# Kernel tuning notes

Measured on AMD Instinct MI355X. Metric: run time of the kernel, lower is better.

## Reference

```python
import jax, jax.numpy as jnp
import numpy as np

HEADS = 4
LOCAL_CTX = 8  # local_attn_ctx (stride)


def _strided_transpose(x, n_ctx, local_ctx):
    # [B, n_ctx, E] -> reshape [B, n_ctx//local, local, E] -> swap -> [B, n_ctx, E]
    B, _, E = x.shape
    bT = n_ctx // local_ctx
    return x.reshape(B, bT, local_ctx, E).transpose(0, 2, 1, 3).reshape(B, n_ctx, E)


def _strided_untranspose(a, n_ctx, local_ctx):
    B, _, E = a.shape
    bT = n_ctx // local_ctx
    return a.reshape(B, local_ctx, bT, E).transpose(0, 2, 1, 3).reshape(B, n_ctx, E)


def setup_inputs() -> dict:
    key = jax.random.key(0)
    ks = jax.random.split(key, 6)
    B, T, E = 2048, 64, 256
    value = jax.random.normal(ks[0], (B, T, E), dtype=jnp.float32)
    k_in = jax.random.normal(ks[1], (B, T, E), dtype=jnp.float32)
    query = jax.random.normal(ks[2], (B, T, E), dtype=jnp.float32)
    mask = jnp.ones((B, T), dtype=jnp.int32)  # unused by the block
    W_ff = jax.random.normal(ks[3], (256, T * E), dtype=jnp.float32) * (1.0 / np.sqrt(T * E))
    b_ff = jax.random.normal(ks[4], (256,), dtype=jnp.float32) * 0.01
    return {"value": value, "key": k_in, "query": query, "mask": mask, "W_ff": W_ff, "b_ff": b_ff}


def reference(value, key, query, mask, W_ff, b_ff):
    B, n_ctx, E = query.shape
    # strided transpose of q, k, v
    q = _strided_transpose(query, n_ctx, LOCAL_CTX)
    k = _strided_transpose(key, n_ctx, LOCAL_CTX)
    v = _strided_transpose(value, n_ctx, LOCAL_CTX)
    scale = 1.0 / np.sqrt(E // HEADS)  # n_state = embd // heads
    w = jax.nn.softmax(jnp.einsum('bqe,bke->bqk', q, k) * scale, axis=-1)
    a = jnp.einsum('bqk,bke->bqe', w, v)
    attention = _strided_untranspose(a, n_ctx, LOCAL_CTX)
    # residual + dropout (eval-mode identity)
    x = attention + query
    # flatten-linear + ReLU
    out = jax.nn.relu(x.reshape(B, n_ctx * E) @ W_ff.T + b_ff)
    return (out, attention)
```

## Files before the change

### kernel.cpp

```cpp
#include <hip/hip_runtime.h>
#include <stdint.h>

typedef __attribute__((ext_vector_type(8))) short s16x8;
typedef __attribute__((ext_vector_type(4))) float f32x4;

__device__ __forceinline__ unsigned short f2bf(float f) {
  unsigned int u = __float_as_uint(f);
  u += 0x7fffu + ((u >> 16) & 1u);
  return (unsigned short)(u >> 16);
}
__device__ __forceinline__ float bf2f(unsigned short h) {
  return __uint_as_float(((unsigned int)h) << 16);
}
__device__ __forceinline__ unsigned short hi_trunc(float f) {
  return (unsigned short)(__float_as_uint(f) >> 16);
}
__device__ __forceinline__ f32x4 mfma16(s16x8 a, s16x8 b, f32x4 c) {
  return __builtin_amdgcn_mfma_f32_16x16x32_bf16(a, b, c, 0, 0, 0);
}

__global__ __launch_bounds__(256, 4) void attn_kernel(
    const float* __restrict__ Vg, const float* __restrict__ Kg,
    const float* __restrict__ Qg, float* __restrict__ attn_out,
    unsigned short* __restrict__ xb ) {
  __shared__ __align__(16) char smem[40960];
  char* PLB = smem + 32768;

  const int b = blockIdx.x;
  const int tid = threadIdx.x;
  const int lane = tid & 63;
  const int w = tid >> 6;
  const int n = lane & 15;
  const int q = lane >> 4;

  const float* Qb = Qg + (size_t)b * 64 * 256;
  const float* Kb = Kg + (size_t)b * 64 * 256;
  const float* Vb = Vg + (size_t)b * 64 * 256;

  const int ve = tid & 127;
  const int vt0 = tid >> 7;

  f32x4 accS[4];
#pragma unroll
  for (int c = 0; c < 4; ++c) accS[c] = f32x4{0.f, 0.f, 0.f, 0.f};

  for (int ph = 0; ph < 2; ++ph) {
    const int e0 = ph * 128;
    float vr[4][8];
#pragma unroll
    for (int i = 0; i < 4; ++i) {
      int tg = i * 2 + vt0;
#pragma unroll
      for (int j = 0; j < 8; ++j) vr[i][j] = Vb[(tg * 8 + j) * 256 + e0 + ve];
    }
#pragma unroll
    for (int kk = 0; kk < 4; ++kk) {
      const int cb = kk * 32 + q * 8;
      const float* qsrc = Qb + (16 * w + n) * 256 + e0 + cb;
      float4 q0 = *(const float4*)qsrc;
      float4 q1 = *(const float4*)(qsrc + 4);
      float4 k0[4], k1[4];
#pragma unroll
      for (int c = 0; c < 4; ++c) {
        const float* ksrc = Kb + (16 * c + n) * 256 + e0 + cb;
        k0[c] = *(const float4*)ksrc;
        k1[c] = *(const float4*)(ksrc + 4);
      }
      float qa[8] = {q0.x, q0.y, q0.z, q0.w, q1.x, q1.y, q1.z, q1.w};
      s16x8 qh, ql;
#pragma unroll
      for (int j = 0; j < 8; ++j) {
        unsigned short h = hi_trunc(qa[j]);
        qh[j] = (short)h;
        ql[j] = (short)f2bf(qa[j] - bf2f(h));
      }
#pragma unroll
      for (int c = 0; c < 4; ++c) {
        float ka[8] = {k0[c].x, k0[c].y, k0[c].z, k0[c].w,
                       k1[c].x, k1[c].y, k1[c].z, k1[c].w};
        s16x8 kh, kl;
#pragma unroll
        for (int j = 0; j < 8; ++j) {
          unsigned short h = hi_trunc(ka[j]);
          kh[j] = (short)h;
          kl[j] = (short)f2bf(ka[j] - bf2f(h));
        }
        accS[c] = mfma16(qh, kh, accS[c]);
        accS[c] = mfma16(qh, kl, accS[c]);
        accS[c] = mfma16(ql, kh, accS[c]);
      }
    }
#pragma unroll
    for (int i = 0; i < 4; ++i) {
      int tg = i * 2 + vt0;
      int e = e0 + ve;
      s16x8 pk;
#pragma unroll
      for (int j = 0; j < 8; ++j) pk[j] = (short)f2bf(vr[i][j]);
      *(s16x8*)(smem + e * 128 + ((tg * 16) ^ ((e & 7) << 4))) = pk;
    }
  }

  const float scale = 0.125f;
  float p[4][4];
#pragma unroll
  for (int r = 0; r < 4; ++r) {
    float m = -1e30f;
#pragma unroll
    for (int c = 0; c < 4; ++c) m = fmaxf(m, accS[c][r]);
#pragma unroll
    for (int mk = 1; mk < 16; mk <<= 1) m = fmaxf(m, __shfl_xor(m, mk, 64));
    float s = 0.f;
#pragma unroll
    for (int c = 0; c < 4; ++c) {
      float e = __expf((accS[c][r] - m) * scale);
      p[c][r] = e;
      s += e;
    }
#pragma unroll
    for (int mk = 1; mk < 16; mk <<= 1) s += __shfl_xor(s, mk, 64);
    float inv = 1.0f / s;
#pragma unroll
    for (int c = 0; c < 4; ++c) p[c][r] *= inv;
  }

#pragma unroll
  for (int r = 0; r < 4; ++r) {
    int row = 16 * w + 4 * q + r;
    int sw = (row & 7) << 4;
#pragma unroll
    for (int c = 0; c < 4; ++c)
      *(unsigned short*)(PLB + row * 128 + ((2 * (16 * c + n)) ^ sw)) =
          f2bf(p[c][r]);
  }
  __syncthreads();

  f32x4 accA[16];
#pragma unroll
  for (int c = 0; c < 16; ++c) accA[c] = f32x4{0.f, 0.f, 0.f, 0.f};
  __builtin_amdgcn_s_setprio(1);
#pragma unroll
  for (int ks = 0; ks < 2; ++ks) {
    const int cb = (ks * 32 + q * 8) * 2;
    const int sw = (n & 7) << 4;
    s16x8 af = *(const s16x8*)(PLB + (16 * w + n) * 128 + (cb ^ sw));
#pragma unroll
    for (int c = 0; c < 16; ++c) {
      int row = 16 * c + n;
      s16x8 bf = *(const s16x8*)(smem + row * 128 + (cb ^ sw));
      accA[c] = mfma16(af, bf, accA[c]);
    }
  }
  __builtin_amdgcn_s_setprio(0);

  if (xb) {
#pragma unroll
    for (int h = 0; h < 2; ++h) {
      __syncthreads();
#pragma unroll
      for (int r = 0; r < 4; ++r) {
        int t = 16 * w + 4 * q + r;
        int sw = (t & 7) << 4;
#pragma unroll
        for (int c8 = 0; c8 < 8; ++c8) {
          int el = 16 * c8 + n;
          *(float*)(smem + t * 512 + ((el * 4) ^ sw)) = accA[h * 8 + c8][r];
        }
      }
      __syncthreads();
#pragma unroll
      for (int i = 0; i < 8; ++i) {
        int f4 = i * 256 + tid;
        int row = f4 >> 5;
        int col4 = f4 & 31;
        int e = h * 128 + col4 * 4;
        float4 av = *(const float4*)(smem + row * 512 + ((col4 * 16) ^ ((row & 7) << 4)));
        float4 qv = *(const float4*)(Qb + row * 256 + e);
        size_t base = ((size_t)b * 64 + row) * 256 + e;
        *(float4*)(attn_out + base) = av;
        ushort4 o;
        o.x = f2bf(av.x + qv.x);
        o.y = f2bf(av.y + qv.y);
        o.z = f2bf(av.z + qv.z);
        o.w = f2bf(av.w + qv.w);
        *(ushort4*)(xb + base) = o;
      }
    }
  } else {
#pragma unroll
    for (int r = 0; r < 4; ++r) {
      int t = 16 * w + 4 * q + r;
      size_t base = ((size_t)b * 64 + t) * 256;
#pragma unroll
      for (int c = 0; c < 16; ++c) attn_out[base + 16 * c + n] = accA[c][r];
    }
  }
}

__global__ __launch_bounds__(256) void w2b_kernel(const float* __restrict__ W,
                                                  unsigned short* __restrict__ Wb) {
  int i = blockIdx.x * 256 + threadIdx.x;
  float4 v = ((const float4*)W)[i];
  ushort4 o;
  o.x = f2bf(v.x); o.y = f2bf(v.y); o.z = f2bf(v.z); o.w = f2bf(v.w);
  ((ushort4*)Wb)[i] = o;
}

template <bool USE_XB>
__global__ __launch_bounds__(256) void ff_kernel(
    const unsigned short* __restrict__ xb, const float* __restrict__ attn,
    const float* __restrict__ query, const unsigned short* __restrict__ Wb,
    float* __restrict__ part, int kchunk) {
  __shared__ __align__(16) unsigned short As[64 * 72];
  __shared__ __align__(16) unsigned short Bs[64 * 72];
  const int tid = threadIdx.x;
  const int lane = tid & 63, w = tid >> 6, n = lane & 15, q = lane >> 4;
  const int m0 = blockIdx.x * 64;
  const int n0 = blockIdx.y * 64;
  const int k0 = blockIdx.z * kchunk;

  f32x4 acc[4];
#pragma unroll
  for (int c = 0; c < 4; ++c) acc[c] = f32x4{0.f, 0.f, 0.f, 0.f};

  const int srow = tid >> 3;
  const int scol = (tid & 7) * 8;

  for (int kk = 0; kk < kchunk; kk += 64) {
#pragma unroll
    for (int rr = 0; rr < 2; ++rr) {
      int row = rr * 32 + srow;
      size_t ga = (size_t)(m0 + row) * 16384 + k0 + kk + scol;
      if (USE_XB) {
        *(uint4*)(As + row * 72 + scol) = *(const uint4*)(xb + ga);
      } else {
        float4 a0 = *(const float4*)(attn + ga);
        float4 a1 = *(const float4*)(attn + ga + 4);
        float4 q0 = *(const float4*)(query + ga);
        float4 q1 = *(const float4*)(query + ga + 4);
        ushort4 h0, h1;
        h0.x = f2bf(a0.x + q0.x); h0.y = f2bf(a0.y + q0.y);
        h0.z = f2bf(a0.z + q0.z); h0.w = f2bf(a0.w + q0.w);
        h1.x = f2bf(a1.x + q1.x); h1.y = f2bf(a1.y + q1.y);
        h1.z = f2bf(a1.z + q1.z); h1.w = f2bf(a1.w + q1.w);
        *(ushort4*)(As + row * 72 + scol) = h0;
        *(ushort4*)(As + row * 72 + scol + 4) = h1;
      }
      size_t gw = (size_t)(n0 + row) * 16384 + k0 + kk + scol;
      *(uint4*)(Bs + row * 72 + scol) = *(const uint4*)(Wb + gw);
    }
    __syncthreads();
#pragma unroll
    for (int ks = 0; ks < 2; ++ks) {
      const int colb = ks * 32 + q * 8;
      s16x8 af = *(const s16x8*)(As + (16 * w + n) * 72 + colb);
#pragma unroll
      for (int c = 0; c < 4; ++c) {
        s16x8 bf = *(const s16x8*)(Bs + (16 * c + n) * 72 + colb);
        acc[c] = mfma16(af, bf, acc[c]);
      }
    }
    __syncthreads();
  }
#pragma unroll
  for (int r = 0; r < 4; ++r) {
    int m = m0 + 16 * w + 4 * q + r;
#pragma unroll
    for (int c = 0; c < 4; ++c) {
      int nn = n0 + 16 * c + n;
      part[((size_t)blockIdx.z * 2048 + m) * 256 + nn] = acc[c][r];
    }
  }
}

__global__ __launch_bounds__(256) void relu_kernel(const float* __restrict__ part,
                                                   const float* __restrict__ bias,
                                                   float* __restrict__ out, int KS) {
  int idx = blockIdx.x * 256 + threadIdx.x;
  float s = bias[idx & 255];
  for (int ks = 0; ks < KS; ++ks) s += part[(size_t)ks * 2048 * 256 + idx];
  out[idx] = fmaxf(s, 0.f);
}

extern "C" void kernel_launch(void* const* d_in, const int* in_sizes, int n_in,
                              void* d_out, int out_size, void* d_ws, size_t ws_size,
                              hipStream_t stream) {
  const float* value = (const float*)d_in[0];
  const float* key   = (const float*)d_in[1];
  const float* query = (const float*)d_in[2];
  const float* W_ff  = (const float*)d_in[4];
  const float* b_ff  = (const float*)d_in[5];

  float* out  = (float*)d_out;
  float* attn = out + (size_t)2048 * 256;

  const int KS = 4;
  const size_t wb_bytes   = (size_t)256 * 16384 * 2;
  const size_t part_bytes = (size_t)KS * 2048 * 256 * 4;
  const size_t xb_bytes   = (size_t)2048 * 64 * 256 * 2;
  unsigned short* Wb = (unsigned short*)d_ws;
  float* part = (float*)((char*)d_ws + wb_bytes);
  bool use_xb = ws_size >= wb_bytes + part_bytes + xb_bytes;
  unsigned short* xb =
      use_xb ? (unsigned short*)((char*)d_ws + wb_bytes + part_bytes) : nullptr;

  w2b_kernel<<<4096, 256, 0, stream>>>(W_ff, Wb);
  attn_kernel<<<2048, 256, 0, stream>>>(value, key, query, attn, xb);
  dim3 gb(32, 4, KS);
  if (use_xb)
    ff_kernel<true><<<gb, 256, 0, stream>>>(xb, nullptr, nullptr, Wb, part, 16384 / KS);
  else
    ff_kernel<false><<<gb, 256, 0, stream>>>(nullptr, attn, query, Wb, part, 16384 / KS);
  relu_kernel<<<2048, 256, 0, stream>>>(part, b_ff, out, KS);
}
```

Before: 317.3 us.

## Stream V through smaller LDS in quarter chunks and write outputs directly

The attention kernel no longer stages all of V (bf16) in a 32KB LDS buffer. It loads V in four 64-column quarters into an 8KB buffer, prefetching the next quarters into registers while the PV MFMAs for the current quarter run. The epilogue drops the LDS transpose and writes attn_out and the bf16 residual directly with per-element stores. LDS use falls from 40KB to 16KB and the min-blocks launch bound is removed, which should raise occupancy. The cost is extra barriers per quarter and narrower, less coalesced global stores.

```diff
diff --git a/kernel.cpp b/kernel.cpp
--- a/kernel.cpp
+++ b/kernel.cpp
@@ -19,12 +19,24 @@
   return __builtin_amdgcn_mfma_f32_16x16x32_bf16(a, b, c, 0, 0, 0);
 }
 
-__global__ __launch_bounds__(256, 4) void attn_kernel(
+__device__ __forceinline__ void write_vq(char* VqB, int ep2, int tg, const float2* g) {
+  s16x8 lo, hi;
+#pragma unroll
+  for (int j = 0; j < 8; ++j) {
+    lo[j] = (short)f2bf(g[j].x);
+    hi[j] = (short)f2bf(g[j].y);
+  }
+  *(s16x8*)(VqB + ep2 * 128 + ((16 * tg) ^ (((ep2 >> 1) & 7) << 4))) = lo;
+  *(s16x8*)(VqB + (ep2 + 1) * 128 + ((16 * tg) ^ (((ep2 >> 1) & 7) << 4))) = hi;
+}
+
+__global__ __launch_bounds__(256) void attn_kernel(
     const float* __restrict__ Vg, const float* __restrict__ Kg,
     const float* __restrict__ Qg, float* __restrict__ attn_out,
     unsigned short* __restrict__ xb ) {
-  __shared__ __align__(16) char smem[40960];
-  char* PLB = smem + 32768;
+  __shared__ __align__(16) char smem[16384];
+  char* VqB = smem;
+  char* PLB = smem + 8192;
 
   const int b = blockIdx.x;
   const int tid = threadIdx.x;
@@ -37,22 +49,16 @@
   const float* Kb = Kg + (size_t)b * 64 * 256;
   const float* Vb = Vg + (size_t)b * 64 * 256;
 
-  const int ve = tid & 127;
-  const int vt0 = tid >> 7;
+  const int ep2 = (tid & 31) * 2;
+  const int tg = tid >> 5;
 
   f32x4 accS[4];
 #pragma unroll
   for (int c = 0; c < 4; ++c) accS[c] = f32x4{0.f, 0.f, 0.f, 0.f};
 
+#pragma unroll
   for (int ph = 0; ph < 2; ++ph) {
     const int e0 = ph * 128;
-    float vr[4][8];
-#pragma unroll
-    for (int i = 0; i < 4; ++i) {
-      int tg = i * 2 + vt0;
-#pragma unroll
-      for (int j = 0; j < 8; ++j) vr[i][j] = Vb[(tg * 8 + j) * 256 + e0 + ve];
-    }
 #pragma unroll
     for (int kk = 0; kk < 4; ++kk) {
       const int cb = kk * 32 + q * 8;
@@ -90,16 +96,15 @@
         accS[c] = mfma16(ql, kh, accS[c]);
       }
     }
-#pragma unroll
-    for (int i = 0; i < 4; ++i) {
-      int tg = i * 2 + vt0;
-      int e = e0 + ve;
-      s16x8 pk;
-#pragma unroll
-      for (int j = 0; j < 8; ++j) pk[j] = (short)f2bf(vr[i][j]);
-      *(s16x8*)(smem + e * 128 + ((tg * 16) ^ ((e & 7) << 4))) = pk;
-    }
-  }
+    if (ph == 0) {
+    }
+  }
+
+  float2 g0[8], g1[8];
+#pragma unroll
+  for (int j = 0; j < 8; ++j) g0[j] = *(const float2*)(Vb + (tg * 8 + j) * 256 + 0 + ep2);
+#pragma unroll
+  for (int j = 0; j < 8; ++j) g1[j] = *(const float2*)(Vb + (tg * 8 + j) * 256 + 64 + ep2);
 
   const float scale = 0.125f;
   float p[4][4];
@@ -133,66 +138,61 @@
       *(unsigned short*)(PLB + row * 128 + ((2 * (16 * c + n)) ^ sw)) =
           f2bf(p[c][r]);
   }
+
+  write_vq(VqB, ep2, tg, g0);
   __syncthreads();
 
-  f32x4 accA[16];
-#pragma unroll
-  for (int c = 0; c < 16; ++c) accA[c] = f32x4{0.f, 0.f, 0.f, 0.f};
-  __builtin_amdgcn_s_setprio(1);
-#pragma unroll
-  for (int ks = 0; ks < 2; ++ks) {
-    const int cb = (ks * 32 + q * 8) * 2;
-    const int sw = (n & 7) << 4;
-    s16x8 af = *(const s16x8*)(PLB + (16 * w + n) * 128 + (cb ^ sw));
-#pragma unroll
-    for (int c = 0; c < 16; ++c) {
-      int row = 16 * c + n;
-      s16x8 bf = *(const s16x8*)(smem + row * 128 + (cb ^ sw));
-      accA[c] = mfma16(af, bf, accA[c]);
-    }
-  }
-  __builtin_amdgcn_s_setprio(0);
-
-  if (xb) {
-#pragma unroll
-    for (int h = 0; h < 2; ++h) {
-      __syncthreads();
-#pragma unroll
-      for (int r = 0; r < 4; ++r) {
-        int t = 16 * w + 4 * q + r;
-        int sw = (t & 7) << 4;
-#pragma unroll
-        for (int c8 = 0; c8 < 8; ++c8) {
-          int el = 16 * c8 + n;
-          *(float*)(smem + t * 512 + ((el * 4) ^ sw)) = accA[h * 8 + c8][r];
-        }
-      }
-      __syncthreads();
-#pragma unroll
-      for (int i = 0; i < 8; ++i) {
-        int f4 = i * 256 + tid;
-        int row = f4 >> 5;
-        int col4 = f4 & 31;
-        int e = h * 128 + col4 * 4;
-        float4 av = *(const float4*)(smem + row * 512 + ((col4 * 16) ^ ((row & 7) << 4)));
-        float4 qv = *(const float4*)(Qb + row * 256 + e);
-        size_t base = ((size_t)b * 64 + row) * 256 + e;
-        *(float4*)(attn_out + base) = av;
-        ushort4 o;
-        o.x = f2bf(av.x + qv.x);
-        o.y = f2bf(av.y + qv.y);
-        o.z = f2bf(av.z + qv.z);
-        o.w = f2bf(av.w + qv.w);
-        *(ushort4*)(xb + base) = o;
-      }
-    }
-  } else {
+  float2 g2[8], g3[8];
+#pragma unroll
+  for (int qi = 0; qi < 4; ++qi) {
+    if (qi == 0) {
+#pragma unroll
+      for (int j = 0; j < 8; ++j)
+        g2[j] = *(const float2*)(Vb + (tg * 8 + j) * 256 + 128 + ep2);
+    }
+    if (qi == 1) {
+#pragma unroll
+      for (int j = 0; j < 8; ++j)
+        g3[j] = *(const float2*)(Vb + (tg * 8 + j) * 256 + 192 + ep2);
+    }
+
+    f32x4 accA[4];
+#pragma unroll
+    for (int c = 0; c < 4; ++c) accA[c] = f32x4{0.f, 0.f, 0.f, 0.f};
+    __builtin_amdgcn_s_setprio(1);
+#pragma unroll
+    for (int ks = 0; ks < 2; ++ks) {
+      const int cb = (ks * 32 + q * 8) * 2;
+      s16x8 af = *(const s16x8*)(PLB + (16 * w + n) * 128 + (cb ^ ((n & 7) << 4)));
+#pragma unroll
+      for (int c = 0; c < 4; ++c) {
+        int row = 16 * c + n;
+        s16x8 bf = *(const s16x8*)(VqB + row * 128 + (cb ^ (((row >> 1) & 7) << 4)));
+        accA[c] = mfma16(af, bf, accA[c]);
+      }
+    }
+    __builtin_amdgcn_s_setprio(0);
+
 #pragma unroll
     for (int r = 0; r < 4; ++r) {
       int t = 16 * w + 4 * q + r;
-      size_t base = ((size_t)b * 64 + t) * 256;
-#pragma unroll
-      for (int c = 0; c < 16; ++c) attn_out[base + 16 * c + n] = accA[c][r];
+      const float* qrow = Qb + t * 256 + qi * 64;
+      size_t base = ((size_t)b * 64 + t) * 256 + qi * 64;
+#pragma unroll
+      for (int c = 0; c < 4; ++c) {
+        int e = 16 * c + n;
+        float aval = accA[c][r];
+        attn_out[base + e] = aval;
+        if (xb) xb[base + e] = f2bf(aval + qrow[e]);
+      }
+    }
+
+    if (qi < 3) {
+      __syncthreads();
+      if (qi == 0) write_vq(VqB, ep2, tg, g1);
+      if (qi == 1) write_vq(VqB, ep2, tg, g2);
+      if (qi == 2) write_vq(VqB, ep2, tg, g3);
+      __syncthreads();
     }
   }
 }
```

New measurement: 292.0 us. 1.09x faster.
